# Kernel optimization log

Hardware: AMD Instinct MI355X
Metric: run time of the kernel (lower is better)

Reference implementation:

```python
import jax, jax.numpy as jnp
import numpy as np

N, E, T = 6144, 98304, 32
D_IN, D, D_FF, H, OUT = 128, 256, 256, 4, 2
DH = D // H
EPS = 1e-5


def setup_inputs() -> dict:
    key = jax.random.key(0)
    ks = jax.random.split(key, 24)
    s = 0.05
    inp = {
        "x": jax.random.normal(ks[0], (N, D_IN), jnp.float32),
        "edge_index": jax.random.randint(ks[1], (2, E), 0, N, jnp.int64 if jax.config.jax_enable_x64 else jnp.int32),
        "timesteps": jnp.sort(jax.random.randint(ks[2], (N,), 0, T)),
        "lin_l_w": jax.random.normal(ks[3], (D, D_IN), jnp.float32) * s,
        "lin_l_b": jnp.zeros((D,), jnp.float32),
        "lin_r_w": jax.random.normal(ks[4], (D, D_IN), jnp.float32) * s,
        "bn_gamma": jnp.ones((D,), jnp.float32),
        "bn_beta": jnp.zeros((D,), jnp.float32),
        "in_proj_w": jax.random.normal(ks[5], (2, 3 * D, D), jnp.float32) * s,
        "in_proj_b": jnp.zeros((2, 3 * D), jnp.float32),
        "out_w": jax.random.normal(ks[6], (2, D, D), jnp.float32) * s,
        "out_b": jnp.zeros((2, D), jnp.float32),
        "ff1_w": jax.random.normal(ks[7], (2, D_FF, D), jnp.float32) * s,
        "ff1_b": jnp.zeros((2, D_FF), jnp.float32),
        "ff2_w": jax.random.normal(ks[8], (2, D, D_FF), jnp.float32) * s,
        "ff2_b": jnp.zeros((2, D), jnp.float32),
        "ln1_g": jnp.ones((2, D), jnp.float32),
        "ln1_b": jnp.zeros((2, D), jnp.float32),
        "ln2_g": jnp.ones((2, D), jnp.float32),
        "ln2_b": jnp.zeros((2, D), jnp.float32),
        "cls_w": jax.random.normal(ks[9], (OUT, D), jnp.float32) * s,
        "cls_b": jnp.zeros((OUT,), jnp.float32),
    }
    return inp


def _layernorm(h, g, b):
    mu = jnp.mean(h, -1, keepdims=True)
    v = jnp.var(h, -1, keepdims=True)
    return (h - mu) * jax.lax.rsqrt(v + EPS) * g + b


def _forward(x, edge_index, timesteps, lin_l_w, lin_l_b, lin_r_w, bn_gamma, bn_beta,
             in_proj_w, in_proj_b, out_w, out_b, ff1_w, ff1_b, ff2_w, ff2_b,
             ln1_g, ln1_b, ln2_g, ln2_b, cls_w, cls_b):
    # SAGEConv (mean aggregation): out = lin_l(mean_{j->i} x_j) + lin_r(x_i)
    src, dst = edge_index[0], edge_index[1]
    agg = jax.ops.segment_sum(x[src], dst, num_segments=N)
    cnt = jax.ops.segment_sum(jnp.ones((E,), x.dtype), dst, num_segments=N)
    agg = agg / jnp.maximum(cnt, 1.0)[:, None]
    h = agg @ lin_l_w.T + lin_l_b + x @ lin_r_w.T

    # BatchNorm1d (training batch stats) + ReLU
    mu = jnp.mean(h, 0)
    var = jnp.var(h, 0)
    h = (h - mu) * jax.lax.rsqrt(var + EPS) * bn_gamma + bn_beta
    h = jax.nn.relu(h)

    # Per-timestep transformer == full attention with block-diagonal mask
    mask = timesteps[:, None] == timesteps[None, :]  # [N, N]
    neg = jnp.finfo(h.dtype).min

    for l in range(2):
        # self-attention (post-norm TransformerEncoderLayer)
        qkv = h @ in_proj_w[l].T + in_proj_b[l]             # [N, 3D]
        q, k, v = jnp.split(qkv, 3, axis=-1)
        q = q.reshape(N, H, DH).transpose(1, 0, 2)          # [H, N, DH]
        k = k.reshape(N, H, DH).transpose(1, 0, 2)
        v = v.reshape(N, H, DH).transpose(1, 0, 2)
        scores = jnp.einsum('hnd,hmd->hnm', q, k) / jnp.sqrt(jnp.asarray(DH, h.dtype))
        scores = jnp.where(mask[None], scores, neg)
        attn = jax.nn.softmax(scores, axis=-1)
        o = jnp.einsum('hnm,hmd->hnd', attn, v).transpose(1, 0, 2).reshape(N, D)
        o = o @ out_w[l].T + out_b[l]
        h = _layernorm(h + o, ln1_g[l], ln1_b[l])
        # FFN
        f = jax.nn.relu(h @ ff1_w[l].T + ff1_b[l]) @ ff2_w[l].T + ff2_b[l]
        h = _layernorm(h + f, ln2_g[l], ln2_b[l])

    return h @ cls_w.T + cls_b  # [N, OUT]


def reference(x, edge_index, timesteps, lin_l_w, lin_l_b, lin_r_w, bn_gamma, bn_beta,
              in_proj_w, in_proj_b, out_w, out_b, ff1_w, ff1_b, ff2_w, ff2_b,
              ln1_g, ln1_b, ln2_g, ln2_b, cls_w, cls_b):
    return _forward(x, edge_index, timesteps, lin_l_w, lin_l_b, lin_r_w, bn_gamma, bn_beta,
                    in_proj_w, in_proj_b, out_w, out_b, ff1_w, ff1_b, ff2_w, ff2_b,
                    ln1_g, ln1_b, ln2_g, ln2_b, cls_w, cls_b)
```

## Files before the change

### kernel.cpp

```cpp
#include <hip/hip_runtime.h>

#define NN   6144
#define EE   98304
#define DIN  128
#define DD   256
#define TT   32
#define NH   4
#define ATTN_Z 6
#define WROWS 3328

typedef __attribute__((ext_vector_type(8))) short short8;
typedef __attribute__((ext_vector_type(4))) float f32x4;
typedef unsigned short u16;

__device__ __forceinline__ float bf2f(u16 u) {
    return __uint_as_float(((unsigned)u) << 16);
}
__device__ __forceinline__ u16 f2bf(float f) {
    unsigned u = __float_as_uint(f);
    return (u16)((u + 0x7fffu + ((u >> 16) & 1u)) >> 16);
}
__device__ __forceinline__ unsigned pk2(float a, float b) {
    return (unsigned)f2bf(a) | ((unsigned)f2bf(b) << 16);
}

__global__ void aml_hist_k(const int* __restrict__ ei, int* __restrict__ deg) {
    int e = blockIdx.x * 256 + threadIdx.x;
    if (e < EE) atomicAdd(&deg[ei[EE + e]], 1);
}

__global__ void aml_scan_k(const int* __restrict__ deg, int* __restrict__ rowptr,
                           int* __restrict__ cursor) {
    int t = threadIdx.x;
    int base = t * 24;
    int loc[24];
    int s = 0;
    #pragma unroll
    for (int j = 0; j < 24; ++j) { loc[j] = s; s += deg[base + j]; }
    __shared__ int part[256];
    part[t] = s;
    __syncthreads();
    for (int o = 1; o < 256; o <<= 1) {
        int v = (t >= o) ? part[t - o] : 0;
        __syncthreads();
        part[t] += v;
        __syncthreads();
    }
    int off = (t > 0) ? part[t - 1] : 0;
    #pragma unroll
    for (int j = 0; j < 24; ++j) {
        rowptr[base + j] = off + loc[j];
        cursor[base + j] = off + loc[j];
    }
    if (t == 255) rowptr[NN] = part[255];
}

__global__ void aml_scatter2_k(const int* __restrict__ ei, int* __restrict__ cursor,
                               int* __restrict__ eid) {
    int e = blockIdx.x * 256 + threadIdx.x;
    if (e >= EE) return;
    int slot = atomicAdd(&cursor[ei[EE + e]], 1);
    eid[slot] = ei[e];
}

__global__ void aml_gather_k(const float* __restrict__ x, const int* __restrict__ rowptr,
                             const int* __restrict__ eid, u16* __restrict__ ac) {
    int node = blockIdx.x * 4 + (threadIdx.x >> 6);
    int lane = threadIdx.x & 63;
    int p0 = rowptr[node], p1 = rowptr[node + 1];
    float ax = 0.f, ay = 0.f;
    int j = p0;
    for (; j + 1 < p1; j += 2) {
        int s0 = eid[j], s1 = eid[j + 1];
        float2 v0 = *(const float2*)(x + (size_t)s0 * DIN + lane * 2);
        float2 v1 = *(const float2*)(x + (size_t)s1 * DIN + lane * 2);
        ax += v0.x + v1.x; ay += v0.y + v1.y;
    }
    if (j < p1) {
        float2 v = *(const float2*)(x + (size_t)eid[j] * DIN + lane * 2);
        ax += v.x; ay += v.y;
    }
    float inv = 1.0f / fmaxf((float)(p1 - p0), 1.0f);
    float2 xr = *(const float2*)(x + (size_t)node * DIN + lane * 2);
    *(unsigned*)(ac + (size_t)node * DD + lane * 2) = pk2(ax * inv, ay * inv);
    *(unsigned*)(ac + (size_t)node * DD + DIN + lane * 2) = pk2(xr.x, xr.y);
}

__global__ void aml_prep_k(const float* __restrict__ lin_l_w, const float* __restrict__ lin_r_w,
                           const float* __restrict__ inp_w, const float* __restrict__ out_w,
                           const float* __restrict__ ff1_w, const float* __restrict__ ff2_w,
                           const int* __restrict__ ts, u16* __restrict__ wb,
                           int* __restrict__ offs) {
    int r = blockIdx.x;
    if (r == WROWS) {
        int t = threadIdx.x;
        if (t <= TT) {
            int lo = 0, hi = NN;
            while (lo < hi) { int mid = (lo + hi) >> 1; if (ts[mid] < t) lo = mid + 1; else hi = mid; }
            offs[t] = lo;
        }
        return;
    }
    int k = threadIdx.x;
    float v;
    if (r < 256) {
        v = (k < DIN) ? lin_l_w[r * DIN + k] : lin_r_w[r * DIN + (k - DIN)];
    } else {
        int r2 = r - 256;
        int l = r2 / 1536, r3 = r2 % 1536;
        const float* src; int rr;
        if (r3 < 768)       { src = inp_w + (size_t)l * 768 * DD; rr = r3; }
        else if (r3 < 1024) { src = out_w + (size_t)l * DD * DD;  rr = r3 - 768; }
        else if (r3 < 1280) { src = ff1_w + (size_t)l * DD * DD;  rr = r3 - 1024; }
        else                { src = ff2_w + (size_t)l * DD * DD;  rr = r3 - 1280; }
        v = src[(size_t)rr * DD + k];
    }
    wb[(size_t)r * DD + k] = f2bf(v);
}

template <int RELU, int AF32, int CF32>
__global__ __launch_bounds__(256)
void aml_gemm_k(const void* __restrict__ A, const u16* __restrict__ Wb,
                const float* __restrict__ bias, void* __restrict__ C, int M) {
    __shared__ __align__(16) unsigned char lds[65536];
    const int t = threadIdx.x;
    const int brow = blockIdx.x * 64;
    const int bcol = blockIdx.y * 64;

    const u16* srcW = Wb + (size_t)bcol * 256;
    #pragma unroll
    for (int p = 0; p < 8; ++p) {
        int c = t + p * 256;
        int row = c >> 5;
        int colb = (c & 31) * 16;
        int dst = row * 512 + (colb ^ ((row & 7) << 4));
        if (AF32) {
            const float* sA = (const float*)A + (size_t)(brow + row) * 256 + (c & 31) * 8;
            float4 a0 = *(const float4*)sA;
            float4 a1 = *(const float4*)(sA + 4);
            uint4 pa = { pk2(a0.x, a0.y), pk2(a0.z, a0.w), pk2(a1.x, a1.y), pk2(a1.z, a1.w) };
            *(uint4*)(lds + dst) = pa;
        } else {
            const u16* sA = (const u16*)A + (size_t)(brow + row) * 256 + (c & 31) * 8;
            *(uint4*)(lds + dst) = *(const uint4*)sA;
        }
        *(uint4*)(lds + 32768 + dst) = *(const uint4*)(srcW + (size_t)row * 256 + (c & 31) * 8);
    }
    __syncthreads();

    const int wave = t >> 6, lane = t & 63;
    const int lrow = lane & 15, lk = lane >> 4;
    const int arow = wave * 16 + lrow;
    f32x4 acc[4] = {};
    #pragma unroll
    for (int ks = 0; ks < 8; ++ks) {
        int kbyte = ks * 64 + lk * 16;
        short8 af = *(const short8*)(lds + arow * 512 + (kbyte ^ ((arow & 7) << 4)));
        #pragma unroll
        for (int ct = 0; ct < 4; ++ct) {
            int wrow = ct * 16 + lrow;
            short8 bf = *(const short8*)(lds + 32768 + wrow * 512 + (kbyte ^ ((wrow & 7) << 4)));
            acc[ct] = __builtin_amdgcn_mfma_f32_16x16x32_bf16(af, bf, acc[ct], 0, 0, 0);
        }
    }

    #pragma unroll
    for (int ct = 0; ct < 4; ++ct) {
        int col = bcol + ct * 16 + lrow;
        float bv = bias[col];
        #pragma unroll
        for (int r = 0; r < 4; ++r) {
            int grow = brow + wave * 16 + lk * 4 + r;
            float v = acc[ct][r] + bv;
            if (RELU) v = fmaxf(v, 0.0f);
            if (CF32) ((float*)C)[(size_t)grow * M + col] = v;
            else      ((u16*)C)[(size_t)grow * M + col] = f2bf(v);
        }
    }
}

__global__ void aml_bn_stats_k(const float* __restrict__ h, float* __restrict__ stats) {
    int d = threadIdx.x;
    int r0 = blockIdx.x * 96;
    float s = 0.f, ss = 0.f;
    for (int i = 0; i < 96; ++i) {
        float v = h[(size_t)(r0 + i) * DD + d];
        s += v; ss += v * v;
    }
    atomicAdd(&stats[d], s);
    atomicAdd(&stats[DD + d], ss);
}

__global__ void aml_bn_apply_k(float* __restrict__ h, const float* __restrict__ stats,
                               const float* __restrict__ g, const float* __restrict__ b) {
    int idx = blockIdx.x * 256 + threadIdx.x;
    int d = idx & (DD - 1);
    float mu = stats[d] * (1.0f / NN);
    float var = stats[DD + d] * (1.0f / NN) - mu * mu;
    float v = (h[idx] - mu) * rsqrtf(var + 1e-5f) * g[d] + b[d];
    h[idx] = fmaxf(v, 0.0f);
}

__global__ __launch_bounds__(256)
void aml_attn_k(const u16* __restrict__ qkv, const int* __restrict__ offs,
                u16* __restrict__ o) {
    int tb = blockIdx.x, head = blockIdx.y, z = blockIdx.z;
    int start = offs[tb], end = offs[tb + 1];
    int S = end - start;
    if (S <= z * 64) return;
    int t = threadIdx.x, wave = t >> 6, lane = t & 63;
    int lq = lane & 15, lk = lane >> 4;
    int qoff = head * 64;

    __shared__ __align__(16) unsigned char Kl[8192];
    __shared__ __align__(16) unsigned char Vt[8192];
    __shared__ __align__(16) unsigned char Pl[4][2048];
    __shared__ float Ol[4][16][65];

    int qi = start + z * 64 + wave * 16 + lq;
    int qic = min(qi, end - 1);
    const u16* qp = qkv + (size_t)qic * 768 + qoff + lk * 8;
    short8 qf[2];
    qf[0] = *(const short8*)qp;
    qf[1] = *(const short8*)(qp + 32);

    float m = -1e30f, l = 0.f;
    f32x4 acc[4] = {};

    int ntile = (S + 63) >> 6;
    for (int tile = 0; tile < ntile; ++tile) {
        int jcnt = S - tile * 64; if (jcnt > 64) jcnt = 64;
        {
            int j = t >> 2, d0 = (t & 3) * 16;
            unsigned char* krow = Kl + j * 128;
            if (j < jcnt) {
                const u16* kp = qkv + (size_t)(start + tile * 64 + j) * 768 + 256 + qoff + d0;
                *(uint4*)(krow + ((d0 * 2) ^ ((j & 7) << 4))) = *(const uint4*)kp;
                *(uint4*)(krow + ((d0 * 2 + 16) ^ ((j & 7) << 4))) = *(const uint4*)(kp + 8);
                const u16* vp = kp + 256;
                #pragma unroll
                for (int i = 0; i < 16; ++i) {
                    int d = d0 + i;
                    *(u16*)(Vt + d * 128 + ((j * 2) ^ ((d & 7) << 4))) = vp[i];
                }
            } else {
                uint4 zz = { 0, 0, 0, 0 };
                *(uint4*)(krow + ((d0 * 2) ^ ((j & 7) << 4))) = zz;
                *(uint4*)(krow + ((d0 * 2 + 16) ^ ((j & 7) << 4))) = zz;
                #pragma unroll
                for (int i = 0; i < 16; ++i) {
                    int d = d0 + i;
                    *(u16*)(Vt + d * 128 + ((j * 2) ^ ((d & 7) << 4))) = 0;
                }
            }
        }
        __syncthreads();

        f32x4 sv[4];
        #pragma unroll
        for (int kt = 0; kt < 4; ++kt) {
            int kr = kt * 16 + lq;
            f32x4 s = {};
            #pragma unroll
            for (int ks = 0; ks < 2; ++ks) {
                short8 kf = *(const short8*)(Kl + kr * 128 + ((ks * 64 + lk * 16) ^ ((kr & 7) << 4)));
                s = __builtin_amdgcn_mfma_f32_16x16x32_bf16(kf, qf[ks], s, 0, 0, 0);
            }
            sv[kt] = s;
        }
        float pm = -1e30f;
        #pragma unroll
        for (int kt = 0; kt < 4; ++kt) {
            #pragma unroll
            for (int r = 0; r < 4; ++r) {
                int kk = tile * 64 + kt * 16 + lk * 4 + r;
                float s = (kk < S) ? sv[kt][r] * 0.125f : -1e30f;
                sv[kt][r] = s;
                pm = fmaxf(pm, s);
            }
        }
        pm = fmaxf(pm, __shfl_xor(pm, 16));
        pm = fmaxf(pm, __shfl_xor(pm, 32));
        float mn = fmaxf(m, pm);
        float corr = __expf(m - mn);
        m = mn;
        float ps = 0.f;
        #pragma unroll
        for (int kt = 0; kt < 4; ++kt) {
            #pragma unroll
            for (int r = 0; r < 4; ++r) {
                float p = __expf(sv[kt][r] - mn);
                sv[kt][r] = p;
                ps += p;
            }
            uint2 w = { pk2(sv[kt][0], sv[kt][1]), pk2(sv[kt][2], sv[kt][3]) };
            *(uint2*)(Pl[wave] + lq * 128 + ((kt * 32 + lk * 8) ^ ((lq & 7) << 4))) = w;
        }
        ps += __shfl_xor(ps, 16);
        ps += __shfl_xor(ps, 32);
        l = l * corr + ps;
        #pragma unroll
        for (int dt = 0; dt < 4; ++dt) {
            #pragma unroll
            for (int r = 0; r < 4; ++r) acc[dt][r] *= corr;
        }
        #pragma unroll
        for (int ks = 0; ks < 2; ++ks) {
            short8 pf = *(const short8*)(Pl[wave] + lq * 128 + ((ks * 64 + lk * 16) ^ ((lq & 7) << 4)));
            #pragma unroll
            for (int dt = 0; dt < 4; ++dt) {
                int dr = dt * 16 + lq;
                short8 vf = *(const short8*)(Vt + dr * 128 + ((ks * 64 + lk * 16) ^ ((dr & 7) << 4)));
                acc[dt] = __builtin_amdgcn_mfma_f32_16x16x32_bf16(vf, pf, acc[dt], 0, 0, 0);
            }
        }
        __syncthreads();
    }

    float linv = 1.0f / l;
    #pragma unroll
    for (int dt = 0; dt < 4; ++dt) {
        #pragma unroll
        for (int r = 0; r < 4; ++r)
            Ol[wave][lq][dt * 16 + lk * 4 + r] = acc[dt][r] * linv;
    }
    int q2 = lane >> 2, c2 = lane & 3;
    int qg = start + z * 64 + wave * 16 + q2;
    if (qg < end) {
        u16* op = o + (size_t)qg * DD + qoff + c2 * 16;
        const float* sp = &Ol[wave][q2][c2 * 16];
        #pragma unroll
        for (int i = 0; i < 8; ++i)
            ((unsigned*)op)[i] = pk2(sp[2 * i], sp[2 * i + 1]);
    }
}

__global__ void aml_ln_k(float* __restrict__ h, const u16* __restrict__ r,
                         const float* __restrict__ g, const float* __restrict__ b) {
    int row = blockIdx.x * 4 + (threadIdx.x >> 6);
    int lane = threadIdx.x & 63;
    float* hp = h + (size_t)row * DD + lane * 4;
    float4 v = *(const float4*)hp;
    uint2 rv = *(const uint2*)(r + (size_t)row * DD + lane * 4);
    v.x += bf2f((u16)(rv.x & 0xffff));
    v.y += bf2f((u16)(rv.x >> 16));
    v.z += bf2f((u16)(rv.y & 0xffff));
    v.w += bf2f((u16)(rv.y >> 16));
    float s = v.x + v.y + v.z + v.w;
    float ss = v.x * v.x + v.y * v.y + v.z * v.z + v.w * v.w;
    #pragma unroll
    for (int off = 32; off; off >>= 1) {
        s += __shfl_xor(s, off);
        ss += __shfl_xor(ss, off);
    }
    float mu = s * (1.0f / DD);
    float var = ss * (1.0f / DD) - mu * mu;
    float inv = rsqrtf(var + 1e-5f);
    float4 gv = *(const float4*)(g + lane * 4);
    float4 bv = *(const float4*)(b + lane * 4);
    v.x = (v.x - mu) * inv * gv.x + bv.x;
    v.y = (v.y - mu) * inv * gv.y + bv.y;
    v.z = (v.z - mu) * inv * gv.z + bv.z;
    v.w = (v.w - mu) * inv * gv.w + bv.w;
    *(float4*)hp = v;
}

__global__ void aml_cls_k(const float* __restrict__ h, const float* __restrict__ w,
                          const float* __restrict__ b, float* __restrict__ out) {
    int row = blockIdx.x * 4 + (threadIdx.x >> 6);
    int lane = threadIdx.x & 63;
    float4 v = *(const float4*)(h + (size_t)row * DD + lane * 4);
    float4 w0 = *(const float4*)(w + lane * 4);
    float4 w1 = *(const float4*)(w + DD + lane * 4);
    float a0 = v.x * w0.x + v.y * w0.y + v.z * w0.z + v.w * w0.w;
    float a1 = v.x * w1.x + v.y * w1.y + v.z * w1.z + v.w * w1.w;
    #pragma unroll
    for (int off = 32; off; off >>= 1) {
        a0 += __shfl_xor(a0, off);
        a1 += __shfl_xor(a1, off);
    }
    if (lane == 0) {
        out[row * 2]     = a0 + b[0];
        out[row * 2 + 1] = a1 + b[1];
    }
}

extern "C" void kernel_launch(void* const* d_in, const int* in_sizes, int n_in,
                              void* d_out, int out_size, void* d_ws, size_t ws_size,
                              hipStream_t stream) {
    const float* x       = (const float*)d_in[0];
    const int*   ei      = (const int*)d_in[1];
    const int*   ts      = (const int*)d_in[2];
    const float* lin_l_w = (const float*)d_in[3];
    const float* lin_l_b = (const float*)d_in[4];
    const float* lin_r_w = (const float*)d_in[5];
    const float* bn_g    = (const float*)d_in[6];
    const float* bn_b    = (const float*)d_in[7];
    const float* inp_w   = (const float*)d_in[8];
    const float* inp_b   = (const float*)d_in[9];
    const float* out_w   = (const float*)d_in[10];
    const float* out_b   = (const float*)d_in[11];
    const float* ff1_w   = (const float*)d_in[12];
    const float* ff1_b   = (const float*)d_in[13];
    const float* ff2_w   = (const float*)d_in[14];
    const float* ff2_b   = (const float*)d_in[15];
    const float* ln1_g   = (const float*)d_in[16];
    const float* ln1_b   = (const float*)d_in[17];
    const float* ln2_g   = (const float*)d_in[18];
    const float* ln2_b   = (const float*)d_in[19];
    const float* cls_w   = (const float*)d_in[20];
    const float* cls_b   = (const float*)d_in[21];

    float* ws     = (float*)d_ws;
    float* stats  = ws;
    int*   deg    = (int*)(stats + 512);
    int*   rowptr = deg + NN;
    int*   cursor = rowptr + NN + 4;
    int*   eid    = cursor + NN;
    int*   offs   = eid + EE;
    u16*   wb     = (u16*)(offs + 64);
    float* h      = (float*)(wb + (size_t)WROWS * 256);
    u16*   qkv    = (u16*)(h + (size_t)NN * DD);
    u16*   t1     = qkv + (size_t)NN * 768;
    u16*   t2     = t1 + (size_t)NN * DD;
    u16*   ac     = qkv;

    const u16* wb_cat = wb;
    const u16* wb_inp[2] = { wb + (size_t)(256) * 256,        wb + (size_t)(256 + 1536) * 256 };
    const u16* wb_out[2] = { wb + (size_t)(256 + 768) * 256,  wb + (size_t)(256 + 1536 + 768) * 256 };
    const u16* wb_ff1[2] = { wb + (size_t)(256 + 1024) * 256, wb + (size_t)(256 + 1536 + 1024) * 256 };
    const u16* wb_ff2[2] = { wb + (size_t)(256 + 1280) * 256, wb + (size_t)(256 + 1536 + 1280) * 256 };

    hipMemsetAsync(stats, 0, 512 * sizeof(float) + NN * sizeof(int), stream);

    aml_hist_k<<<EE / 256, 256, 0, stream>>>(ei, deg);
    aml_scan_k<<<1, 256, 0, stream>>>(deg, rowptr, cursor);
    aml_scatter2_k<<<EE / 256, 256, 0, stream>>>(ei, cursor, eid);
    aml_gather_k<<<NN / 4, 256, 0, stream>>>(x, rowptr, eid, ac);
    aml_prep_k<<<WROWS + 1, 256, 0, stream>>>(lin_l_w, lin_r_w, inp_w, out_w, ff1_w, ff2_w,
                                              ts, wb, offs);
    aml_gemm_k<0, 0, 1><<<dim3(NN / 64, 4), 256, 0, stream>>>(ac, wb_cat, lin_l_b, h, DD);
    aml_bn_stats_k<<<64, 256, 0, stream>>>(h, stats);
    aml_bn_apply_k<<<(NN * DD) / 256, 256, 0, stream>>>(h, stats, bn_g, bn_b);

    for (int l = 0; l < 2; ++l) {
        aml_gemm_k<0, 1, 0><<<dim3(NN / 64, 12), 256, 0, stream>>>(h, wb_inp[l],
                                                                   inp_b + (size_t)l * 768, qkv, 768);
        aml_attn_k<<<dim3(TT, NH, ATTN_Z), 256, 0, stream>>>(qkv, offs, t1);
        aml_gemm_k<0, 0, 0><<<dim3(NN / 64, 4), 256, 0, stream>>>(t1, wb_out[l],
                                                                  out_b + (size_t)l * DD, t2, DD);
        aml_ln_k<<<NN / 4, 256, 0, stream>>>(h, t2, ln1_g + (size_t)l * DD, ln1_b + (size_t)l * DD);
        aml_gemm_k<1, 1, 0><<<dim3(NN / 64, 4), 256, 0, stream>>>(h, wb_ff1[l],
                                                                  ff1_b + (size_t)l * DD, t1, DD);
        aml_gemm_k<0, 0, 0><<<dim3(NN / 64, 4), 256, 0, stream>>>(t1, wb_ff2[l],
                                                                  ff2_b + (size_t)l * DD, t2, DD);
        aml_ln_k<<<NN / 4, 256, 0, stream>>>(h, t2, ln2_g + (size_t)l * DD, ln2_b + (size_t)l * DD);
    }

    aml_cls_k<<<NN / 4, 256, 0, stream>>>(h, cls_w, cls_b, (float*)d_out);
}
```

Baseline: 163.6 us.

## Fuse residual+LayerNorm and classifier into full-row GEMM epilogues; fold BN stats

Result: no change. 164.6 us (+0.6%).

```diff
diff --git a/kernel.cpp b/kernel.cpp
--- a/kernel.cpp
+++ b/kernel.cpp
@@ -118,10 +118,11 @@
     wb[(size_t)r * DD + k] = f2bf(v);
 }
 
-template <int RELU, int AF32, int CF32>
+template <int RELU, int AF32, int CF32, int BNSTAT>
 __global__ __launch_bounds__(256)
 void aml_gemm_k(const void* __restrict__ A, const u16* __restrict__ Wb,
-                const float* __restrict__ bias, void* __restrict__ C, int M) {
+                const float* __restrict__ bias, void* __restrict__ C, int M,
+                float* __restrict__ stats) {
     __shared__ __align__(16) unsigned char lds[65536];
     const int t = threadIdx.x;
     const int brow = blockIdx.x * 64;
@@ -168,6 +169,7 @@
     for (int ct = 0; ct < 4; ++ct) {
         int col = bcol + ct * 16 + lrow;
         float bv = bias[col];
+        float s = 0.f, q = 0.f;
         #pragma unroll
         for (int r = 0; r < 4; ++r) {
             int grow = brow + wave * 16 + lk * 4 + r;
@@ -175,20 +177,17 @@
             if (RELU) v = fmaxf(v, 0.0f);
             if (CF32) ((float*)C)[(size_t)grow * M + col] = v;
             else      ((u16*)C)[(size_t)grow * M + col] = f2bf(v);
-        }
-    }
-}
-
-__global__ void aml_bn_stats_k(const float* __restrict__ h, float* __restrict__ stats) {
-    int d = threadIdx.x;
-    int r0 = blockIdx.x * 96;
-    float s = 0.f, ss = 0.f;
-    for (int i = 0; i < 96; ++i) {
-        float v = h[(size_t)(r0 + i) * DD + d];
-        s += v; ss += v * v;
-    }
-    atomicAdd(&stats[d], s);
-    atomicAdd(&stats[DD + d], ss);
+            if (BNSTAT) { s += v; q += v * v; }
+        }
+        if (BNSTAT) {
+            s += __shfl_xor(s, 16); s += __shfl_xor(s, 32);
+            q += __shfl_xor(q, 16); q += __shfl_xor(q, 32);
+            if (lk == 0) {
+                atomicAdd(&stats[col], s);
+                atomicAdd(&stats[DD + col], q);
+            }
+        }
+    }
 }
 
 __global__ void aml_bn_apply_k(float* __restrict__ h, const float* __restrict__ stats,
@@ -199,6 +198,142 @@
     float var = stats[DD + d] * (1.0f / NN) - mu * mu;
     float v = (h[idx] - mu) * rsqrtf(var + 1e-5f) * g[d] + b[d];
     h[idx] = fmaxf(v, 0.0f);
+}
+
+template <int CLS>
+__global__ __launch_bounds__(256)
+void aml_mega_k(const u16* __restrict__ A, const u16* __restrict__ Wb,
+                const float* __restrict__ bias, float* __restrict__ h,
+                const float* __restrict__ g, const float* __restrict__ bv,
+                const float* __restrict__ cls_w, const float* __restrict__ cls_b,
+                float* __restrict__ out) {
+    __shared__ __align__(16) unsigned char lds[65536];
+    const int t = threadIdx.x;
+    const int brow = blockIdx.x * 64;
+
+    #pragma unroll
+    for (int p = 0; p < 8; ++p) {
+        int c = t + p * 256;
+        int row = c >> 5;
+        int colb = (c & 31) * 16;
+        int dst = row * 512 + (colb ^ ((row & 7) << 4));
+        const u16* sA = A + (size_t)(brow + row) * 256 + (c & 31) * 8;
+        *(uint4*)(lds + dst) = *(const uint4*)sA;
+    }
+    #pragma unroll
+    for (int p = 0; p < 8; ++p) {
+        int c = t + p * 256;
+        int row = c >> 5;
+        int colb = (c & 31) * 16;
+        int dst = 32768 + row * 512 + (colb ^ ((row & 7) << 4));
+        *(uint4*)(lds + dst) = *(const uint4*)(Wb + (size_t)row * 256 + (c & 31) * 8);
+    }
+    __syncthreads();
+
+    const int wave = t >> 6, lane = t & 63;
+    const int lrow = lane & 15, lk = lane >> 4;
+    const int arow = wave * 16 + lrow;
+
+    short8 af[8];
+    #pragma unroll
+    for (int ks = 0; ks < 8; ++ks) {
+        int kbyte = ks * 64 + lk * 16;
+        af[ks] = *(const short8*)(lds + arow * 512 + (kbyte ^ ((arow & 7) << 4)));
+    }
+
+    f32x4 acc[4][4] = {};
+    for (int cT = 0; cT < 4; ++cT) {
+        if (cT) {
+            __syncthreads();
+            #pragma unroll
+            for (int p = 0; p < 8; ++p) {
+                int c = t + p * 256;
+                int row = c >> 5;
+                int colb = (c & 31) * 16;
+                int dst = 32768 + row * 512 + (colb ^ ((row & 7) << 4));
+                *(uint4*)(lds + dst) = *(const uint4*)(Wb + (size_t)(cT * 64 + row) * 256 + (c & 31) * 8);
+            }
+            __syncthreads();
+        }
+        #pragma unroll
+        for (int ks = 0; ks < 8; ++ks) {
+            int kbyte = ks * 64 + lk * 16;
+            #pragma unroll
+            for (int ct = 0; ct < 4; ++ct) {
+                int wrow = ct * 16 + lrow;
+                short8 bf = *(const short8*)(lds + 32768 + wrow * 512 + (kbyte ^ ((wrow & 7) << 4)));
+                acc[cT][ct] = __builtin_amdgcn_mfma_f32_16x16x32_bf16(af[ks], bf, acc[cT][ct], 0, 0, 0);
+            }
+        }
+    }
+
+    float s[4] = {}, q[4] = {};
+    #pragma unroll
+    for (int cT = 0; cT < 4; ++cT) {
+        #pragma unroll
+        for (int ct = 0; ct < 4; ++ct) {
+            int col = cT * 64 + ct * 16 + lrow;
+            float bvv = bias[col];
+            #pragma unroll
+            for (int r = 0; r < 4; ++r) {
+                int grow = brow + wave * 16 + lk * 4 + r;
+                float v = acc[cT][ct][r] + bvv + h[(size_t)grow * DD + col];
+                acc[cT][ct][r] = v;
+                s[r] += v; q[r] += v * v;
+            }
+        }
+    }
+    #pragma unroll
+    for (int off = 1; off < 16; off <<= 1) {
+        #pragma unroll
+        for (int r = 0; r < 4; ++r) {
+            s[r] += __shfl_xor(s[r], off);
+            q[r] += __shfl_xor(q[r], off);
+        }
+    }
+    float mu[4], iv[4];
+    #pragma unroll
+    for (int r = 0; r < 4; ++r) {
+        mu[r] = s[r] * (1.0f / DD);
+        iv[r] = rsqrtf(q[r] * (1.0f / DD) - mu[r] * mu[r] + 1e-5f);
+    }
+    float c0[4] = {}, c1[4] = {};
+    #pragma unroll
+    for (int cT = 0; cT < 4; ++cT) {
+        #pragma unroll
+        for (int ct = 0; ct < 4; ++ct) {
+            int col = cT * 64 + ct * 16 + lrow;
+            float gv = g[col], bb = bv[col];
+            float w0 = CLS ? cls_w[col] : 0.f;
+            float w1 = CLS ? cls_w[DD + col] : 0.f;
+            #pragma unroll
+            for (int r = 0; r < 4; ++r) {
+                int grow = brow + wave * 16 + lk * 4 + r;
+                float v = (acc[cT][ct][r] - mu[r]) * iv[r] * gv + bb;
+                h[(size_t)grow * DD + col] = v;
+                if (CLS) { c0[r] += v * w0; c1[r] += v * w1; }
+            }
+        }
+    }
+    if (CLS) {
+        #pragma unroll
+        for (int off = 1; off < 16; off <<= 1) {
+            #pragma unroll
+            for (int r = 0; r < 4; ++r) {
+                c0[r] += __shfl_xor(c0[r], off);
+                c1[r] += __shfl_xor(c1[r], off);
+            }
+        }
+        if (lrow == 0) {
+            float cb0 = cls_b[0], cb1 = cls_b[1];
+            #pragma unroll
+            for (int r = 0; r < 4; ++r) {
+                int grow = brow + wave * 16 + lk * 4 + r;
+                out[grow * 2]     = c0[r] + cb0;
+                out[grow * 2 + 1] = c1[r] + cb1;
+            }
+        }
+    }
 }
 
 __global__ __launch_bounds__(256)
@@ -335,56 +470,6 @@
     }
 }
 
-__global__ void aml_ln_k(float* __restrict__ h, const u16* __restrict__ r,
-                         const float* __restrict__ g, const float* __restrict__ b) {
-    int row = blockIdx.x * 4 + (threadIdx.x >> 6);
-    int lane = threadIdx.x & 63;
-    float* hp = h + (size_t)row * DD + lane * 4;
-    float4 v = *(const float4*)hp;
-    uint2 rv = *(const uint2*)(r + (size_t)row * DD + lane * 4);
-    v.x += bf2f((u16)(rv.x & 0xffff));
-    v.y += bf2f((u16)(rv.x >> 16));
-    v.z += bf2f((u16)(rv.y & 0xffff));
-    v.w += bf2f((u16)(rv.y >> 16));
-    float s = v.x + v.y + v.z + v.w;
-    float ss = v.x * v.x + v.y * v.y + v.z * v.z + v.w * v.w;
-    #pragma unroll
-    for (int off = 32; off; off >>= 1) {
-        s += __shfl_xor(s, off);
-        ss += __shfl_xor(ss, off);
-    }
-    float mu = s * (1.0f / DD);
-    float var = ss * (1.0f / DD) - mu * mu;
-    float inv = rsqrtf(var + 1e-5f);
-    float4 gv = *(const float4*)(g + lane * 4);
-    float4 bv = *(const float4*)(b + lane * 4);
-    v.x = (v.x - mu) * inv * gv.x + bv.x;
-    v.y = (v.y - mu) * inv * gv.y + bv.y;
-    v.z = (v.z - mu) * inv * gv.z + bv.z;
-    v.w = (v.w - mu) * inv * gv.w + bv.w;
-    *(float4*)hp = v;
-}
-
-__global__ void aml_cls_k(const float* __restrict__ h, const float* __restrict__ w,
-                          const float* __restrict__ b, float* __restrict__ out) {
-    int row = blockIdx.x * 4 + (threadIdx.x >> 6);
-    int lane = threadIdx.x & 63;
-    float4 v = *(const float4*)(h + (size_t)row * DD + lane * 4);
-    float4 w0 = *(const float4*)(w + lane * 4);
-    float4 w1 = *(const float4*)(w + DD + lane * 4);
-    float a0 = v.x * w0.x + v.y * w0.y + v.z * w0.z + v.w * w0.w;
-    float a1 = v.x * w1.x + v.y * w1.y + v.z * w1.z + v.w * w1.w;
-    #pragma unroll
-    for (int off = 32; off; off >>= 1) {
-        a0 += __shfl_xor(a0, off);
-        a1 += __shfl_xor(a1, off);
-    }
-    if (lane == 0) {
-        out[row * 2]     = a0 + b[0];
-        out[row * 2 + 1] = a1 + b[1];
-    }
-}
-
 extern "C" void kernel_launch(void* const* d_in, const int* in_sizes, int n_in,
                               void* d_out, int out_size, void* d_ws, size_t ws_size,
                               hipStream_t stream) {
@@ -422,7 +507,6 @@
     float* h      = (float*)(wb + (size_t)WROWS * 256);
     u16*   qkv    = (u16*)(h + (size_t)NN * DD);
     u16*   t1     = qkv + (size_t)NN * 768;
-    u16*   t2     = t1 + (size_t)NN * DD;
     u16*   ac     = qkv;
 
     const u16* wb_cat = wb;
@@ -439,23 +523,27 @@
     aml_gather_k<<<NN / 4, 256, 0, stream>>>(x, rowptr, eid, ac);
     aml_prep_k<<<WROWS + 1, 256, 0, stream>>>(lin_l_w, lin_r_w, inp_w, out_w, ff1_w, ff2_w,
                                               ts, wb, offs);
-    aml_gemm_k<0, 0, 1><<<dim3(NN / 64, 4), 256, 0, stream>>>(ac, wb_cat, lin_l_b, h, DD);
-    aml_bn_stats_k<<<64, 256, 0, stream>>>(h, stats);
+    aml_gemm_k<0, 0, 1, 1><<<dim3(NN / 64, 4), 256, 0, stream>>>(ac, wb_cat, lin_l_b, h, DD, stats);
     aml_bn_apply_k<<<(NN * DD) / 256, 256, 0, stream>>>(h, stats, bn_g, bn_b);
 
     for (int l = 0; l < 2; ++l) {
-        aml_gemm_k<0, 1, 0><<<dim3(NN / 64, 12), 256, 0, stream>>>(h, wb_inp[l],
-                                                                   inp_b + (size_t)l * 768, qkv, 768);
+        aml_gemm_k<0, 1, 0, 0><<<dim3(NN / 64, 12), 256, 0, stream>>>(h, wb_inp[l],
+                                                                      inp_b + (size_t)l * 768,
+                                                                      qkv, 768, nullptr);
         aml_attn_k<<<dim3(TT, NH, ATTN_Z), 256, 0, stream>>>(qkv, offs, t1);
-        aml_gemm_k<0, 0, 0><<<dim3(NN / 64, 4), 256, 0, stream>>>(t1, wb_out[l],
-                                                                  out_b + (size_t)l * DD, t2, DD);
-        aml_ln_k<<<NN / 4, 256, 0, stream>>>(h, t2, ln1_g + (size_t)l * DD, ln1_b + (size_t)l * DD);
-        aml_gemm_k<1, 1, 0><<<dim3(NN / 64, 4), 256, 0, stream>>>(h, wb_ff1[l],
-                                                                  ff1_b + (size_t)l * DD, t1, DD);
-        aml_gemm_k<0, 0, 0><<<dim3(NN / 64, 4), 256, 0, stream>>>(t1, wb_ff2[l],
-                                                                  ff2_b + (size_t)l * DD, t2, DD);
-        aml_ln_k<<<NN / 4, 256, 0, stream>>>(h, t2, ln2_g + (size_t)l * DD, ln2_b + (size_t)l * DD);
-    }
-
-    aml_cls_k<<<NN / 4, 256, 0, stream>>>(h, cls_w, cls_b, (float*)d_out);
-}
+        aml_mega_k<0><<<NN / 64, 256, 0, stream>>>(t1, wb_out[l], out_b + (size_t)l * DD, h,
+                                                   ln1_g + (size_t)l * DD, ln1_b + (size_t)l * DD,
+                                                   nullptr, nullptr, nullptr);
+        aml_gemm_k<1, 1, 0, 0><<<dim3(NN / 64, 4), 256, 0, stream>>>(h, wb_ff1[l],
+                                                                     ff1_b + (size_t)l * DD,
+                                                                     t1, DD, nullptr);
+        if (l == 0)
+            aml_mega_k<0><<<NN / 64, 256, 0, stream>>>(t1, wb_ff2[l], ff2_b + (size_t)l * DD, h,
+                                                       ln2_g + (size_t)l * DD, ln2_b + (size_t)l * DD,
+                                                       nullptr, nullptr, nullptr);
+        else
+            aml_mega_k<1><<<NN / 64, 256, 0, stream>>>(t1, wb_ff2[l], ff2_b + (size_t)l * DD, h,
+                                                       ln2_g + (size_t)l * DD, ln2_b + (size_t)l * DD,
+                                                       cls_w, cls_b, (float*)d_out);
+    }
+}
```
